# Performance work log

Hardware: AMD Instinct MI355X
Metric: run time of the kernel (lower is better)

The kernel has to match this reference:

```python
import jax, jax.numpy as jnp
import numpy as np

DN = ('NCHW', 'HWIO', 'NCHW')

def conv_same(x, w):
    # TF 'same' padding for even kernels pads more at the end; lax 'SAME' matches.
    return jax.lax.conv_general_dilated(x, w, (1, 1), 'SAME', dimension_numbers=DN)

def hard_sigmoid(z):
    # Keras hard_sigmoid
    return jnp.clip(0.2 * z + 0.5, 0.0, 1.0)

def setup_inputs() -> dict:
    key = jax.random.key(0)
    k1, k2, k3 = jax.random.split(key, 3)
    B, T, C, H, W = 8, 16, 16, 128, 128
    FILTERS = 2
    x = jax.random.normal(k1, (B, T, C, H, W), jnp.float32)
    # Keras HWIO kernels; 4*filters output channels for i,f,c,o gates
    Wx = jax.random.normal(k2, (4, 2, C, 4 * FILTERS), jnp.float32) * 0.05
    Wh = jax.random.normal(k3, (4, 2, FILTERS, 4 * FILTERS), jnp.float32) * 0.05
    return {"x": x, "Wx": Wx, "Wh": Wh}

def convlstm(x, Wx, Wh):
    B, T, C, H, W = x.shape
    F = Wh.shape[2]  # filters
    # go_backwards=True: process time axis reversed; outputs stay in processed order
    xr = x[:, ::-1]
    # Precompute input convolution for all timesteps in one big conv
    xg = conv_same(xr.reshape(B * T, C, H, W), Wx).reshape(B, T, 4 * F, H, W)
    xg = jnp.moveaxis(xg, 1, 0)  # (T, B, 4F, H, W)
    h0 = jnp.zeros((B, F, H, W), x.dtype)
    c0 = jnp.zeros((B, F, H, W), x.dtype)

    def step(carry, xg_t):
        h, c = carry
        hg = conv_same(h, Wh)  # (B, 4F, H, W)
        xi, xf, xc, xo = jnp.split(xg_t, 4, axis=1)
        hi, hf, hc, ho = jnp.split(hg, 4, axis=1)
        i = hard_sigmoid(xi + hi)
        f = hard_sigmoid(xf + hf)
        c_new = f * c + i * jnp.tanh(xc + hc)
        o = hard_sigmoid(xo + ho)
        h_new = o * jnp.tanh(c_new)
        return (h_new, c_new), h_new

    _, hs = jax.lax.scan(step, (h0, c0), xg)  # hs: (T, B, F, H, W)
    return jnp.moveaxis(hs, 0, 1)  # (B, T, F, H, W)

def reference(x, Wx, Wh):
    return convlstm(x, Wx, Wh)
```

## Files before the change

kernel.cpp:

```cpp
#include <hip/hip_runtime.h>
#include <cmath>


constexpr int B_ = 8;
constexpr int T_ = 16;
constexpr int C_ = 16;
constexpr int F_ = 2;
constexpr int O_ = 8;
constexpr int H_ = 128;
constexpr int W_ = 128;
constexpr int HW_ = H_ * W_;
constexpr int KH_ = 4;
constexpr int KW_ = 2;
constexpr int PX_ = 4;

typedef float fv4 __attribute__((ext_vector_type(4)));

__device__ __forceinline__ float hsig(float z) {
    return fminf(fmaxf(0.2f * z + 0.5f, 0.0f), 1.0f);
}

__device__ __forceinline__ float ftanh(float x) {
    float e = __expf(2.0f * x);
    return fmaf(-2.0f, 1.0f / (e + 1.0f), 1.0f);
}

template<bool CHECK>
__device__ __forceinline__ void conv_body(
    const float* __restrict__ xs,
    const float* __restrict__ Wx,
    float acc[PX_][O_],
    int oh, int ow4, bool cval, int co4)
{
    #pragma unroll 2
    for (int c = 0; c < C_; ++c) {
        const float* xc = xs + c * HW_ + ow4;
        float xv[KH_][PX_ + 1];
        #pragma unroll
        for (int kh = 0; kh < KH_; ++kh) {
            int ih  = oh + kh - 1;
            bool rv = true;
            int ihc = ih;
            if (CHECK) {
                rv  = (unsigned)ih < (unsigned)H_;
                ihc = rv ? ih : 0;
            }
            const float* r = xc + ihc * W_;
            fv4   v  = *reinterpret_cast<const fv4*>(r);
            float t4 = r[co4];
            xv[kh][0] = v.x;
            xv[kh][1] = v.y;
            xv[kh][2] = v.z;
            xv[kh][3] = v.w;
            xv[kh][4] = cval ? t4 : 0.0f;
            if (CHECK) {
                #pragma unroll
                for (int p = 0; p < PX_ + 1; ++p)
                    xv[kh][p] = rv ? xv[kh][p] : 0.0f;
            }
        }
        #pragma unroll
        for (int kh = 0; kh < KH_; ++kh) {
            const float* wp = Wx + kh * (KW_ * C_ * O_) + c * O_;
            #pragma unroll
            for (int o = 0; o < O_; ++o) {
                float w0 = wp[o];
                float w1 = wp[C_ * O_ + o];
                acc[0][o] = fmaf(xv[kh][0], w0, acc[0][o]);
                acc[1][o] = fmaf(xv[kh][1], w0, acc[1][o]);
                acc[2][o] = fmaf(xv[kh][2], w0, acc[2][o]);
                acc[3][o] = fmaf(xv[kh][3], w0, acc[3][o]);
                acc[0][o] = fmaf(xv[kh][1], w1, acc[0][o]);
                acc[1][o] = fmaf(xv[kh][2], w1, acc[1][o]);
                acc[2][o] = fmaf(xv[kh][3], w1, acc[2][o]);
                acc[3][o] = fmaf(xv[kh][4], w1, acc[3][o]);
            }
        }
    }
}

__global__ __launch_bounds__(256, 4) void xg_kernel(
    const float* __restrict__ x,
    const float* __restrict__ Wx,
    float* __restrict__ xg)
{
    int wid = (blockIdx.x & 7) * 256 + (blockIdx.x >> 3);

    int gid = wid * 256 + threadIdx.x;
    int bt  = gid >> 12;
    int rem = gid & 4095;
    int oh  = rem >> 5;
    int ow4 = (rem & 31) << 2;

    int b    = bt >> 4;
    int trev = bt & 15;
    int t    = 15 - trev;

    const float* xs = x + (size_t)bt * C_ * HW_;

    float acc[PX_][O_];
    #pragma unroll
    for (int p = 0; p < PX_; ++p)
        #pragma unroll
        for (int o = 0; o < O_; ++o) acc[p][o] = 0.0f;

    bool cval = ow4 < (W_ - 4);
    int  co4  = cval ? 4 : 0;

    int row0 = ((wid * 256) & 4095) >> 5;
    if (row0 >= 1 && row0 <= 118) {
        conv_body<false>(xs, Wx, acc, oh, ow4, cval, co4);
    } else {
        conv_body<true>(xs, Wx, acc, oh, ow4, cval, co4);
    }

    float* dst = xg + (size_t)(t * B_ + b) * O_ * HW_ + oh * W_ + ow4;
    #pragma unroll
    for (int o = 0; o < O_; ++o) {
        fv4 s;
        s.x = acc[0][o]; s.y = acc[1][o]; s.z = acc[2][o]; s.w = acc[3][o];
        __builtin_nontemporal_store(s, reinterpret_cast<fv4*>(dst + o * HW_));
    }
}

__global__ __launch_bounds__(256) void step_kernel(
    const float* __restrict__ xg,
    const float* __restrict__ Wh,
    float* __restrict__ out,
    float* __restrict__ cbuf,
    int t)
{
    int gid = blockIdx.x * 256 + threadIdx.x;
    int b   = gid >> 14;
    int pix = gid & (HW_ - 1);
    int oh  = pix >> 7;
    int ow  = pix & (W_ - 1);

    const float* xgp = xg + (size_t)(t * B_ + b) * O_ * HW_ + pix;
    float acc[O_];
    #pragma unroll
    for (int o = 0; o < O_; ++o)
        acc[o] = __builtin_nontemporal_load(xgp + o * HW_);

    bool cv  = (ow + 1) < W_;
    int  co1 = cv ? 1 : 0;

    if (t > 0) {
        const float* hs = out + (size_t)(b * T_ + (t - 1)) * F_ * HW_;
        #pragma unroll
        for (int kh = 0; kh < KH_; ++kh) {
            int ih  = oh + kh - 1;
            bool rv = (unsigned)ih < (unsigned)H_;
            int ihc = rv ? ih : 0;
            const float* hrow = hs + ihc * W_ + ow;
            const float* wb   = Wh + kh * (KW_ * F_ * O_);
            #pragma unroll
            for (int f = 0; f < F_; ++f) {
                float h0 = hrow[f * HW_];
                float h1 = hrow[f * HW_ + co1];
                h0 = rv ? h0 : 0.0f;
                h1 = (rv && cv) ? h1 : 0.0f;
                #pragma unroll
                for (int o = 0; o < O_; ++o) {
                    acc[o] = fmaf(h0, wb[f * O_ + o], acc[o]);
                    acc[o] = fmaf(h1, wb[F_ * O_ + f * O_ + o], acc[o]);
                }
            }
        }
    }

    size_t cidx = (size_t)b * F_ * HW_ + pix;
    float cp0 = 0.0f, cp1 = 0.0f;
    if (t > 0) { cp0 = cbuf[cidx]; cp1 = cbuf[cidx + HW_]; }

    float gi0 = hsig(acc[0]);
    float gi1 = hsig(acc[1]);
    float gf0 = hsig(acc[2]);
    float gf1 = hsig(acc[3]);
    float gg0 = ftanh(acc[4]);
    float gg1 = ftanh(acc[5]);
    float go0 = hsig(acc[6]);
    float go1 = hsig(acc[7]);

    float cn0 = gf0 * cp0 + gi0 * gg0;
    float cn1 = gf1 * cp1 + gi1 * gg1;
    cbuf[cidx]       = cn0;
    cbuf[cidx + HW_] = cn1;

    size_t oidx = (size_t)(b * T_ + t) * F_ * HW_ + pix;
    out[oidx]       = go0 * ftanh(cn0);
    out[oidx + HW_] = go1 * ftanh(cn1);
}

extern "C" void kernel_launch(void* const* d_in, const int* in_sizes, int n_in,
                              void* d_out, int out_size, void* d_ws, size_t ws_size,
                              hipStream_t stream) {
    const float* x  = (const float*)d_in[0];
    const float* Wx = (const float*)d_in[1];
    const float* Wh = (const float*)d_in[2];
    float* out  = (float*)d_out;

    float* xg   = (float*)d_ws;
    float* cbuf = (float*)((char*)d_ws + (size_t)64 * 1024 * 1024 + 1024);

    int xg_blocks = (B_ * T_ * HW_ / PX_) / 256;
    xg_kernel<<<xg_blocks, 256, 0, stream>>>(x, Wx, xg);

    int blocks = (B_ * HW_) / 256;
    for (int t = 0; t < T_; ++t) {
        step_kernel<<<blocks, 256, 0, stream>>>(xg, Wh, out, cbuf, t);
    }
}
```

Baseline: 128.2 us.

## Compute two output rows per thread and software-pipeline channel loads in xg conv

Each thread in the input-convolution kernel now computes a 2x4 output tile, loading 5 input rows per channel instead of 4 rows for one output row, which reuses input loads and weight loads across two rows. The channel loop is software-pipelined with a double-buffered register set that prefetches the next channel's rows while the current one accumulates. Grid size is halved and the block-to-slab mapping is rewritten. Register pressure roughly doubles for the accumulators (64 floats), which may reduce occupancy under the 4-blocks-per-SM launch bound or cause spills.

```diff
diff --git a/kernel.cpp b/kernel.cpp
--- a/kernel.cpp
+++ b/kernel.cpp
@@ -13,6 +13,8 @@
 constexpr int KH_ = 4;
 constexpr int KW_ = 2;
 constexpr int PX_ = 4;
+constexpr int RY_ = 2;
+constexpr int NR_ = RY_ + KH_ - 1;
 
 typedef float fv4 __attribute__((ext_vector_type(4)));
 
@@ -26,57 +28,75 @@
 }
 
 template<bool CHECK>
-__device__ __forceinline__ void conv_body(
-    const float* __restrict__ xs,
-    const float* __restrict__ Wx,
-    float acc[PX_][O_],
-    int oh, int ow4, bool cval, int co4)
-{
-    #pragma unroll 2
-    for (int c = 0; c < C_; ++c) {
-        const float* xc = xs + c * HW_ + ow4;
-        float xv[KH_][PX_ + 1];
-        #pragma unroll
-        for (int kh = 0; kh < KH_; ++kh) {
-            int ih  = oh + kh - 1;
-            bool rv = true;
-            int ihc = ih;
-            if (CHECK) {
-                rv  = (unsigned)ih < (unsigned)H_;
-                ihc = rv ? ih : 0;
+__device__ __forceinline__ void load_rows(
+    const float* __restrict__ xc, int r0, bool cval, int co4,
+    float xv[NR_][PX_ + 1])
+{
+    #pragma unroll
+    for (int rr = 0; rr < NR_; ++rr) {
+        int ih  = r0 - 1 + rr;
+        bool v  = true;
+        int ihc = ih;
+        if (CHECK) {
+            v   = (unsigned)ih < (unsigned)H_;
+            ihc = v ? ih : 0;
+        }
+        const float* r = xc + ihc * W_;
+        fv4   a  = *reinterpret_cast<const fv4*>(r);
+        float t4 = r[co4];
+        xv[rr][0] = a.x;
+        xv[rr][1] = a.y;
+        xv[rr][2] = a.z;
+        xv[rr][3] = a.w;
+        xv[rr][4] = cval ? t4 : 0.0f;
+        if (CHECK && !v) {
+            #pragma unroll
+            for (int p = 0; p < PX_ + 1; ++p) xv[rr][p] = 0.0f;
+        }
+    }
+}
+
+__device__ __forceinline__ void accum(
+    const float* __restrict__ wc,
+    const float xv[NR_][PX_ + 1],
+    float acc[RY_][PX_][O_])
+{
+    #pragma unroll
+    for (int kh = 0; kh < KH_; ++kh) {
+        const float* wp = wc + kh * (KW_ * C_ * O_);
+        #pragma unroll
+        for (int o = 0; o < O_; ++o) {
+            float w0 = wp[o];
+            float w1 = wp[C_ * O_ + o];
+            #pragma unroll
+            for (int r = 0; r < RY_; ++r) {
+                #pragma unroll
+                for (int p = 0; p < PX_; ++p) {
+                    acc[r][p][o] = fmaf(xv[kh + r][p],     w0, acc[r][p][o]);
+                    acc[r][p][o] = fmaf(xv[kh + r][p + 1], w1, acc[r][p][o]);
+                }
             }
-            const float* r = xc + ihc * W_;
-            fv4   v  = *reinterpret_cast<const fv4*>(r);
-            float t4 = r[co4];
-            xv[kh][0] = v.x;
-            xv[kh][1] = v.y;
-            xv[kh][2] = v.z;
-            xv[kh][3] = v.w;
-            xv[kh][4] = cval ? t4 : 0.0f;
-            if (CHECK) {
-                #pragma unroll
-                for (int p = 0; p < PX_ + 1; ++p)
-                    xv[kh][p] = rv ? xv[kh][p] : 0.0f;
-            }
-        }
-        #pragma unroll
-        for (int kh = 0; kh < KH_; ++kh) {
-            const float* wp = Wx + kh * (KW_ * C_ * O_) + c * O_;
-            #pragma unroll
-            for (int o = 0; o < O_; ++o) {
-                float w0 = wp[o];
-                float w1 = wp[C_ * O_ + o];
-                acc[0][o] = fmaf(xv[kh][0], w0, acc[0][o]);
-                acc[1][o] = fmaf(xv[kh][1], w0, acc[1][o]);
-                acc[2][o] = fmaf(xv[kh][2], w0, acc[2][o]);
-                acc[3][o] = fmaf(xv[kh][3], w0, acc[3][o]);
-                acc[0][o] = fmaf(xv[kh][1], w1, acc[0][o]);
-                acc[1][o] = fmaf(xv[kh][2], w1, acc[1][o]);
-                acc[2][o] = fmaf(xv[kh][3], w1, acc[2][o]);
-                acc[3][o] = fmaf(xv[kh][4], w1, acc[3][o]);
-            }
-        }
-    }
+        }
+    }
+}
+
+template<bool CHECK>
+__device__ __forceinline__ void conv_pipeline(
+    const float* __restrict__ xs, const float* __restrict__ Wx,
+    int r0, bool cval, int co4, float acc[RY_][PX_][O_], int ow4)
+{
+    float xv[NR_][PX_ + 1], xvn[NR_][PX_ + 1];
+    load_rows<CHECK>(xs + ow4, r0, cval, co4, xv);
+    #pragma unroll 1
+    for (int c = 0; c < C_ - 1; ++c) {
+        load_rows<CHECK>(xs + (c + 1) * HW_ + ow4, r0, cval, co4, xvn);
+        accum(Wx + c * O_, xv, acc);
+        #pragma unroll
+        for (int rr = 0; rr < NR_; ++rr)
+            #pragma unroll
+            for (int p = 0; p < PX_ + 1; ++p) xv[rr][p] = xvn[rr][p];
+    }
+    accum(Wx + (C_ - 1) * O_, xv, acc);
 }
 
 __global__ __launch_bounds__(256, 4) void xg_kernel(
@@ -84,42 +104,51 @@
     const float* __restrict__ Wx,
     float* __restrict__ xg)
 {
-    int wid = (blockIdx.x & 7) * 256 + (blockIdx.x >> 3);
-
-    int gid = wid * 256 + threadIdx.x;
-    int bt  = gid >> 12;
-    int rem = gid & 4095;
-    int oh  = rem >> 5;
-    int ow4 = (rem & 31) << 2;
+    int wid = (blockIdx.x & 7) * 128 + (blockIdx.x >> 3);
+
+    int bt   = wid >> 3;
+    int slab = wid & 7;
+
+    int tid = threadIdx.x;
+    int rp  = tid >> 5;
+    int q   = tid & 31;
+    int ow4 = q << 2;
+
+    int r0 = slab * 16 + rp * 2;
 
     int b    = bt >> 4;
     int trev = bt & 15;
     int t    = 15 - trev;
 
     const float* xs = x + (size_t)bt * C_ * HW_;
-
-    float acc[PX_][O_];
-    #pragma unroll
-    for (int p = 0; p < PX_; ++p)
-        #pragma unroll
-        for (int o = 0; o < O_; ++o) acc[p][o] = 0.0f;
-
     bool cval = ow4 < (W_ - 4);
     int  co4  = cval ? 4 : 0;
 
-    int row0 = ((wid * 256) & 4095) >> 5;
-    if (row0 >= 1 && row0 <= 118) {
-        conv_body<false>(xs, Wx, acc, oh, ow4, cval, co4);
+    float acc[RY_][PX_][O_];
+    #pragma unroll
+    for (int r = 0; r < RY_; ++r)
+        #pragma unroll
+        for (int p = 0; p < PX_; ++p)
+            #pragma unroll
+            for (int o = 0; o < O_; ++o) acc[r][p][o] = 0.0f;
+
+    if (slab >= 1 && slab <= 6) {
+        conv_pipeline<false>(xs, Wx, r0, cval, co4, acc, ow4);
     } else {
-        conv_body<true>(xs, Wx, acc, oh, ow4, cval, co4);
-    }
-
-    float* dst = xg + (size_t)(t * B_ + b) * O_ * HW_ + oh * W_ + ow4;
-    #pragma unroll
-    for (int o = 0; o < O_; ++o) {
-        fv4 s;
-        s.x = acc[0][o]; s.y = acc[1][o]; s.z = acc[2][o]; s.w = acc[3][o];
-        __builtin_nontemporal_store(s, reinterpret_cast<fv4*>(dst + o * HW_));
+        conv_pipeline<true>(xs, Wx, r0, cval, co4, acc, ow4);
+    }
+
+    float* dstb = xg + (size_t)(t * B_ + b) * O_ * HW_ + r0 * W_ + ow4;
+    #pragma unroll
+    for (int r = 0; r < RY_; ++r) {
+        #pragma unroll
+        for (int o = 0; o < O_; ++o) {
+            fv4 s;
+            s.x = acc[r][0][o]; s.y = acc[r][1][o];
+            s.z = acc[r][2][o]; s.w = acc[r][3][o];
+            __builtin_nontemporal_store(
+                s, reinterpret_cast<fv4*>(dstb + o * HW_ + r * W_));
+        }
     }
 }
 
@@ -203,7 +232,7 @@
     float* xg   = (float*)d_ws;
     float* cbuf = (float*)((char*)d_ws + (size_t)64 * 1024 * 1024 + 1024);
 
-    int xg_blocks = (B_ * T_ * HW_ / PX_) / 256;
+    int xg_blocks = (B_ * T_ * HW_ / (PX_ * RY_)) / 256;
     xg_kernel<<<xg_blocks, 256, 0, stream>>>(x, Wx, xg);
 
     int blocks = (B_ * HW_) / 256;
```

New measurement: 226.8 us. 1.77x slower.
